# Kernel tuning notes

Hardware: AMD Instinct MI355X
Metric: run time of the kernel (lower is better)

## Reference

```python
import jax, jax.numpy as jnp
import numpy as np

B, NQ, NK, QS, KS, H, VD = 16, 64, 512, 256, 256, 256, 256


def setup_inputs() -> dict:
    key = jax.random.key(0)
    k1, k2, k3, k4, k5, k6, k7 = jax.random.split(key, 7)
    return {
        "queries": jax.random.normal(k1, (B, NQ, QS), dtype=jnp.float32),
        "keys": jax.random.normal(k2, (B, NK, KS), dtype=jnp.float32),
        "values": jax.random.normal(k3, (B, NK, VD), dtype=jnp.float32),
        "valid_lens": jax.random.randint(k4, (B,), 1, NK + 1, dtype=jnp.int32),
        # learned params (nn.Linear with bias=False): W_q [QS,H], W_k [KS,H], w_v [H]
        "W_q": jax.random.normal(k5, (QS, H), dtype=jnp.float32) / np.sqrt(QS),
        "W_k": jax.random.normal(k6, (KS, H), dtype=jnp.float32) / np.sqrt(KS),
        "w_v": jax.random.normal(k7, (H,), dtype=jnp.float32) / np.sqrt(H),
    }


def reference(queries, keys, values, valid_lens, W_q, W_k, w_v):
    # project: q [B,nq,H], k [B,nk,H]
    q = jnp.einsum("bqd,dh->bqh", queries, W_q)
    k = jnp.einsum("bkd,dh->bkh", keys, W_k)
    # broadcast-add -> tanh -> score reduction via w_v: [B,nq,nk]
    features = jnp.tanh(q[:, :, None, :] + k[:, None, :, :])  # [B,nq,nk,H]
    scores = jnp.einsum("bqkh,h->bqk", features, w_v)
    # masked softmax over keys (positions >= valid_len masked out)
    mask = jnp.arange(scores.shape[-1])[None, None, :] < valid_lens[:, None, None]
    scores = jnp.where(mask, scores, -1e6)
    attn = jax.nn.softmax(scores, axis=-1)
    # weighted sum of values (dropout p=0 / eval mode => identity)
    return jnp.einsum("bqk,bkv->bqv", attn, values)
```

## Files before the change

### kernel.cpp

```cpp
#include <hip/hip_runtime.h>
#include <hip/hip_bf16.h>

#define BB 16
#define NQ 64
#define NK 512
#define HD 256

typedef __attribute__((ext_vector_type(8))) short short8;
typedef __attribute__((ext_vector_type(4))) float f32x4;

__device__ __forceinline__ ushort bf16_rne(float v) {
    unsigned u = __float_as_uint(v);
    return (ushort)((u + 0x7FFFu + ((u >> 16) & 1u)) >> 16);
}
__device__ __forceinline__ float bf16_to_f(ushort h) {
    return __uint_as_float(((unsigned)h) << 16);
}

__global__ __launch_bounds__(256) void wconv(
    const float* __restrict__ wq, const float* __restrict__ wk,
    ushort* __restrict__ wqh, ushort* __restrict__ wql,
    ushort* __restrict__ wkh, ushort* __restrict__ wkl)
{
    int widx = blockIdx.x * 256 + threadIdx.x;
    const float* W; ushort *wh, *wl;
    if (widx < 16384) { W = wq; wh = wqh; wl = wql; }
    else { W = wk; wh = wkh; wl = wkl; widx -= 16384; }
    int n  = widx >> 6;
    int k4 = (widx & 63) * 4;
    ushort hh[4], ll[4];
    #pragma unroll
    for (int c = 0; c < 4; ++c) {
        float v = W[(k4 + c) * 256 + n];
        hh[c] = bf16_rne(v);
        ll[c] = bf16_rne(v - bf16_to_f(hh[c]));
    }
    *(ushort4*)&wh[n * 256 + k4] = make_ushort4(hh[0], hh[1], hh[2], hh[3]);
    *(ushort4*)&wl[n * 256 + k4] = make_ushort4(ll[0], ll[1], ll[2], ll[3]);
}

__global__ __launch_bounds__(256, 2) void proj_fused(
    const float* __restrict__ queries, const float* __restrict__ keys,
    const ushort* __restrict__ wqh, const ushort* __restrict__ wql,
    const ushort* __restrict__ wkh, const ushort* __restrict__ wkl,
    float* __restrict__ qp, float* __restrict__ kp, float scale)
{
    __shared__ ushort AsH[64 * 64], AsL[64 * 64];
    __shared__ ushort BsH[64 * 64], BsL[64 * 64];

    const float* A; const ushort *Bh, *Bl; float* C; int rows0;
    const int bx = blockIdx.x;
    if (bx < 16) { A = queries; Bh = wqh; Bl = wql; C = qp; rows0 = bx * 64; }
    else         { A = keys;    Bh = wkh; Bl = wkl; C = kp; rows0 = (bx - 16) * 64; }
    const int cols0 = blockIdx.y * 64;

    const int t = threadIdx.x, lane = t & 63, wave = t >> 6;
    const int quad = lane >> 4, l15 = lane & 15;
    const int sr  = t >> 2;
    const int sc2 = (t & 3) * 2;

    f32x4 acc[4];
    #pragma unroll
    for (int j = 0; j < 4; ++j) acc[j] = (f32x4){0.f, 0.f, 0.f, 0.f};

    for (int k0 = 0; k0 < 256; k0 += 64) {
        const float* arow = &A[(size_t)(rows0 + sr) * 256 + k0 + sc2 * 8];
        float4 a0 = *(const float4*)&arow[0];
        float4 a1 = *(const float4*)&arow[4];
        float4 a2 = *(const float4*)&arow[8];
        float4 a3 = *(const float4*)&arow[12];
        const ushort* bhp = &Bh[(size_t)(cols0 + sr) * 256 + k0 + sc2 * 8];
        const ushort* blp = &Bl[(size_t)(cols0 + sr) * 256 + k0 + sc2 * 8];
        short8 b0h = *(const short8*)&bhp[0];
        short8 b1h = *(const short8*)&bhp[8];
        short8 b0l = *(const short8*)&blp[0];
        short8 b1l = *(const short8*)&blp[8];

        __syncthreads();

        float av[16] = {a0.x, a0.y, a0.z, a0.w, a1.x, a1.y, a1.z, a1.w,
                        a2.x, a2.y, a2.z, a2.w, a3.x, a3.y, a3.z, a3.w};
        short8 ah0, ah1, al0, al1;
        #pragma unroll
        for (int e = 0; e < 8; ++e) {
            ushort h0 = bf16_rne(av[e]);
            ushort h1 = bf16_rne(av[8 + e]);
            ah0[e] = (short)h0;
            ah1[e] = (short)h1;
            al0[e] = (short)bf16_rne(av[e] - bf16_to_f(h0));
            al1[e] = (short)bf16_rne(av[8 + e] - bf16_to_f(h1));
        }
        {
            int s0 = sr * 8 + ((sc2 + 0) ^ (sr & 7));
            int s1 = sr * 8 + ((sc2 + 1) ^ (sr & 7));
            *(short8*)&AsH[s0 * 8] = ah0;
            *(short8*)&AsH[s1 * 8] = ah1;
            *(short8*)&AsL[s0 * 8] = al0;
            *(short8*)&AsL[s1 * 8] = al1;
            *(short8*)&BsH[s0 * 8] = b0h;
            *(short8*)&BsH[s1 * 8] = b1h;
            *(short8*)&BsL[s0 * 8] = b0l;
            *(short8*)&BsL[s1 * 8] = b1l;
        }
        __syncthreads();

        #pragma unroll
        for (int ks = 0; ks < 2; ++ks) {
            const int c = ks * 4 + quad;
            short8 aH, aL, bH[4], bL[4];
            {
                int r = wave * 16 + l15;
                int slot = r * 8 + (c ^ (r & 7));
                aH = *(const short8*)&AsH[slot * 8];
                aL = *(const short8*)&AsL[slot * 8];
            }
            #pragma unroll
            for (int ns = 0; ns < 4; ++ns) {
                int n = ns * 16 + l15;
                int slot = n * 8 + (c ^ (n & 7));
                bH[ns] = *(const short8*)&BsH[slot * 8];
                bL[ns] = *(const short8*)&BsL[slot * 8];
            }
            #pragma unroll
            for (int ns = 0; ns < 4; ++ns)
                acc[ns] = __builtin_amdgcn_mfma_f32_16x16x32_bf16(aH, bH[ns], acc[ns], 0, 0, 0);
            #pragma unroll
            for (int ns = 0; ns < 4; ++ns)
                acc[ns] = __builtin_amdgcn_mfma_f32_16x16x32_bf16(aL, bH[ns], acc[ns], 0, 0, 0);
            #pragma unroll
            for (int ns = 0; ns < 4; ++ns)
                acc[ns] = __builtin_amdgcn_mfma_f32_16x16x32_bf16(aH, bL[ns], acc[ns], 0, 0, 0);
        }
    }

    const int rbase = rows0 + wave * 16 + quad * 4;
    #pragma unroll
    for (int ns = 0; ns < 4; ++ns) {
        int col = cols0 + ns * 16 + l15;
        #pragma unroll
        for (int r = 0; r < 4; ++r)
            C[(size_t)(rbase + r) * 256 + col] =
                __builtin_amdgcn_exp2f(acc[ns][r] * scale);
    }
}

__global__ __launch_bounds__(256, 4) void score_a(
    const float* __restrict__ qp,
    const float* __restrict__ kp,
    const int*   __restrict__ vlens,
    const float* __restrict__ w_v,
    float* __restrict__ Pt)
{
    __shared__ float eq[8][260];
    __shared__ float wv[HD];

    const int b   = blockIdx.x & 15;
    const int qt  = blockIdx.x >> 4;
    const int seg = blockIdx.y;
    const int vl  = vlens[b];
    if (seg * 64 >= vl) return;

    const int t = threadIdx.x, lane = t & 63, wave = t >> 6;
    const int key = wave * 16 + (lane >> 2);
    const int ch  = lane & 3;
    const int kg  = seg * 64 + key;

    const float* krow = kp + ((size_t)b * NK + kg) * HD + ch * 4;
    float4 ek[16];
    #pragma unroll
    for (int j = 0; j < 16; ++j) ek[j] = *(const float4*)&krow[j * 16];

    const float* qsrc = qp + ((size_t)b * NQ + qt * 8) * HD;
    #pragma unroll
    for (int i = 0; i < 2; ++i) {
        int idx = i * 256 + t;
        int row = idx >> 6, c4 = (idx & 63) * 4;
        *(float4*)&eq[row][c4] = *(const float4*)&qsrc[(size_t)row * HD + c4];
    }
    if (t < 64) *(float4*)&wv[t * 4] = *(const float4*)&w_v[t * 4];
    __syncthreads();

    float Wsum;
    {
        float ws = wv[lane] + wv[lane + 64] + wv[lane + 128] + wv[lane + 192];
        #pragma unroll
        for (int off = 32; off; off >>= 1) ws += __shfl_xor(ws, off);
        Wsum = ws;
    }

    float s[8] = {0.f, 0.f, 0.f, 0.f, 0.f, 0.f, 0.f, 0.f};
    #pragma unroll
    for (int j = 0; j < 16; ++j) {
        const int h = j * 16 + ch * 4;
        float4 e4 = ek[j];
        float4 w4 = *(const float4*)&wv[h];
        #pragma unroll
        for (int qi = 0; qi < 8; ++qi) {
            float4 q4 = *(const float4*)&eq[qi][h];
            float p0 = fmaf(q4.x, e4.x, 1.f);
            float p1 = fmaf(q4.y, e4.y, 1.f);
            float p2 = fmaf(q4.z, e4.z, 1.f);
            float p3 = fmaf(q4.w, e4.w, 1.f);
            float d01 = p0 * p1;
            float d23 = p2 * p3;
            float n01 = fmaf(w4.x, p1, w4.y * p0);
            float n23 = fmaf(w4.z, p3, w4.w * p2);
            float num = fmaf(d01, n23, d23 * n01);
            float r   = __builtin_amdgcn_rcpf(d01 * d23);
            s[qi] = fmaf(num, r, s[qi]);
        }
    }
    #pragma unroll
    for (int qi = 0; qi < 8; ++qi) {
        s[qi] += __shfl_xor(s[qi], 1);
        s[qi] += __shfl_xor(s[qi], 2);
    }

    if (ch == 0) {
        const bool masked = (kg >= vl);
        const float L2E = 1.4426950408889634f;
        float pt[8];
        #pragma unroll
        for (int qi = 0; qi < 8; ++qi) {
            float sv = fmaf(-2.f, s[qi], Wsum);
            pt[qi] = masked ? 0.f : __builtin_amdgcn_exp2f(sv * L2E);
        }
        float* dst = &Pt[((size_t)b * NK + kg) * 64 + qt * 8];
        *(float4*)&dst[0] = make_float4(pt[0], pt[1], pt[2], pt[3]);
        *(float4*)&dst[4] = make_float4(pt[4], pt[5], pt[6], pt[7]);
    }
}

__global__ __launch_bounds__(256) void pv_b(
    const float* __restrict__ Pt,
    const float* __restrict__ values,
    const int*   __restrict__ vlens,
    float* __restrict__ out)
{
    __shared__ f32x4 red[128];
    __shared__ float Lred[8];
    __shared__ float Lfin[8];

    const int bx  = blockIdx.x;
    const int b   = bx & 15;
    const int qt  = (bx >> 4) & 7;
    const int vdq = bx >> 7;
    const int vl  = vlens[b];
    const int nk  = ((vl + 63) >> 6) << 6;

    const int t   = threadIdx.x;
    const int vd4 = t & 15;
    const int q   = (t >> 4) & 7;
    const int kp2 = t >> 7;

    const float* vptr = values + (size_t)b * NK * HD + vdq * 64 + vd4 * 4;
    const float* pptr = Pt + (size_t)b * NK * 64 + qt * 8 + q;

    f32x4 acc = (f32x4){0.f, 0.f, 0.f, 0.f};
    float Lacc = 0.f;
    #pragma unroll 8
    for (int k = kp2; k < nk; k += 2) {
        float  p = pptr[(size_t)k * 64];
        float4 v = *(const float4*)&vptr[(size_t)k * HD];
        acc[0] = fmaf(p, v.x, acc[0]);
        acc[1] = fmaf(p, v.y, acc[1]);
        acc[2] = fmaf(p, v.z, acc[2]);
        acc[3] = fmaf(p, v.w, acc[3]);
        Lacc += p;
    }

    if (kp2 == 1) {
        red[t - 128] = acc;
        if (vd4 == 0) Lred[q] = Lacc;
    }
    __syncthreads();
    if (kp2 == 0) {
        f32x4 o = red[t];
        acc[0] += o[0]; acc[1] += o[1]; acc[2] += o[2]; acc[3] += o[3];
        if (vd4 == 0) Lfin[q] = Lacc + Lred[q];
    }
    __syncthreads();
    if (kp2 == 0) {
        float r = __builtin_amdgcn_rcpf(Lfin[q]);
        float4 o = make_float4(acc[0] * r, acc[1] * r, acc[2] * r, acc[3] * r);
        *(float4*)&out[((size_t)(b * 64 + qt * 8 + q)) * 256 + vdq * 64 + vd4 * 4] = o;
    }
}

extern "C" void kernel_launch(void* const* d_in, const int* in_sizes, int n_in,
                              void* d_out, int out_size, void* d_ws, size_t ws_size,
                              hipStream_t stream) {
    const float* queries = (const float*)d_in[0];
    const float* keys    = (const float*)d_in[1];
    const float* values  = (const float*)d_in[2];
    const int*   vlens   = (const int*)d_in[3];
    const float* W_q     = (const float*)d_in[4];
    const float* W_k     = (const float*)d_in[5];
    const float* w_v     = (const float*)d_in[6];
    float* out = (float*)d_out;

    float*  kp  = (float*)d_ws;
    float*  qp  = kp + (size_t)BB * NK * HD;
    float*  Pt  = qp + (size_t)BB * NQ * HD;
    ushort* wqh = (ushort*)(Pt + (size_t)BB * NK * 64);
    ushort* wql = wqh + 65536;
    ushort* wkh = wql + 65536;
    ushort* wkl = wkh + 65536;

    const float SC = 2.885390081777927f;

    wconv<<<dim3(128), 256, 0, stream>>>(W_q, W_k, wqh, wql, wkh, wkl);
    proj_fused<<<dim3(144, 4), 256, 0, stream>>>(queries, keys,
                                                 wqh, wql, wkh, wkl,
                                                 qp, kp, SC);
    score_a<<<dim3(128, 8), 256, 0, stream>>>(qp, kp, vlens, w_v, Pt);
    pv_b<<<dim3(512), 256, 0, stream>>>(Pt, values, vlens, out);
}
```

Baseline: 123.0 us.

## Fuse weight bf16 split into projection GEMM and software-pipeline PV loads

Removes the separate wconv launch. The projection kernel now reads fp32 W_q/W_k directly with strided loads and splits them into bf16 hi/lo inside the tile-staging step. This saves a kernel launch and a workspace round-trip, but each of the 144x4 blocks redoes the conversion and uses uncoalesced column reads of W. Separately, the PV kernel's loop is rewritten as a register double-buffered pipeline that prefetches 8 rows of P and V ahead, to hide global load latency.

```diff
diff --git a/kernel.cpp b/kernel.cpp
--- a/kernel.cpp
+++ b/kernel.cpp
@@ -17,41 +17,18 @@
     return __uint_as_float(((unsigned)h) << 16);
 }
 
-__global__ __launch_bounds__(256) void wconv(
-    const float* __restrict__ wq, const float* __restrict__ wk,
-    ushort* __restrict__ wqh, ushort* __restrict__ wql,
-    ushort* __restrict__ wkh, ushort* __restrict__ wkl)
-{
-    int widx = blockIdx.x * 256 + threadIdx.x;
-    const float* W; ushort *wh, *wl;
-    if (widx < 16384) { W = wq; wh = wqh; wl = wql; }
-    else { W = wk; wh = wkh; wl = wkl; widx -= 16384; }
-    int n  = widx >> 6;
-    int k4 = (widx & 63) * 4;
-    ushort hh[4], ll[4];
-    #pragma unroll
-    for (int c = 0; c < 4; ++c) {
-        float v = W[(k4 + c) * 256 + n];
-        hh[c] = bf16_rne(v);
-        ll[c] = bf16_rne(v - bf16_to_f(hh[c]));
-    }
-    *(ushort4*)&wh[n * 256 + k4] = make_ushort4(hh[0], hh[1], hh[2], hh[3]);
-    *(ushort4*)&wl[n * 256 + k4] = make_ushort4(ll[0], ll[1], ll[2], ll[3]);
-}
-
-__global__ __launch_bounds__(256, 2) void proj_fused(
+__global__ __launch_bounds__(256, 2) void proj_fused2(
     const float* __restrict__ queries, const float* __restrict__ keys,
-    const ushort* __restrict__ wqh, const ushort* __restrict__ wql,
-    const ushort* __restrict__ wkh, const ushort* __restrict__ wkl,
+    const float* __restrict__ W_q, const float* __restrict__ W_k,
     float* __restrict__ qp, float* __restrict__ kp, float scale)
 {
     __shared__ ushort AsH[64 * 64], AsL[64 * 64];
     __shared__ ushort BsH[64 * 64], BsL[64 * 64];
 
-    const float* A; const ushort *Bh, *Bl; float* C; int rows0;
+    const float* A; const float* W; float* C; int rows0;
     const int bx = blockIdx.x;
-    if (bx < 16) { A = queries; Bh = wqh; Bl = wql; C = qp; rows0 = bx * 64; }
-    else         { A = keys;    Bh = wkh; Bl = wkl; C = kp; rows0 = (bx - 16) * 64; }
+    if (bx < 16) { A = queries; W = W_q; C = qp; rows0 = bx * 64; }
+    else         { A = keys;    W = W_k; C = kp; rows0 = (bx - 16) * 64; }
     const int cols0 = blockIdx.y * 64;
 
     const int t = threadIdx.x, lane = t & 63, wave = t >> 6;
@@ -69,18 +46,19 @@
         float4 a1 = *(const float4*)&arow[4];
         float4 a2 = *(const float4*)&arow[8];
         float4 a3 = *(const float4*)&arow[12];
-        const ushort* bhp = &Bh[(size_t)(cols0 + sr) * 256 + k0 + sc2 * 8];
-        const ushort* blp = &Bl[(size_t)(cols0 + sr) * 256 + k0 + sc2 * 8];
-        short8 b0h = *(const short8*)&bhp[0];
-        short8 b1h = *(const short8*)&bhp[8];
-        short8 b0l = *(const short8*)&blp[0];
-        short8 b1l = *(const short8*)&blp[8];
+        float wvv[16];
+        {
+            const float* wsrc = &W[(size_t)(k0 + sc2 * 8) * 256 + cols0 + sr];
+            #pragma unroll
+            for (int e = 0; e < 16; ++e)
+                wvv[e] = wsrc[(size_t)e * 256];
+        }
 
         __syncthreads();
 
         float av[16] = {a0.x, a0.y, a0.z, a0.w, a1.x, a1.y, a1.z, a1.w,
                         a2.x, a2.y, a2.z, a2.w, a3.x, a3.y, a3.z, a3.w};
-        short8 ah0, ah1, al0, al1;
+        short8 ah0, ah1, al0, al1, bh0, bh1, bl0, bl1;
         #pragma unroll
         for (int e = 0; e < 8; ++e) {
             ushort h0 = bf16_rne(av[e]);
@@ -89,6 +67,12 @@
             ah1[e] = (short)h1;
             al0[e] = (short)bf16_rne(av[e] - bf16_to_f(h0));
             al1[e] = (short)bf16_rne(av[8 + e] - bf16_to_f(h1));
+            ushort w0 = bf16_rne(wvv[e]);
+            ushort w1 = bf16_rne(wvv[8 + e]);
+            bh0[e] = (short)w0;
+            bh1[e] = (short)w1;
+            bl0[e] = (short)bf16_rne(wvv[e] - bf16_to_f(w0));
+            bl1[e] = (short)bf16_rne(wvv[8 + e] - bf16_to_f(w1));
         }
         {
             int s0 = sr * 8 + ((sc2 + 0) ^ (sr & 7));
@@ -97,10 +81,10 @@
             *(short8*)&AsH[s1 * 8] = ah1;
             *(short8*)&AsL[s0 * 8] = al0;
             *(short8*)&AsL[s1 * 8] = al1;
-            *(short8*)&BsH[s0 * 8] = b0h;
-            *(short8*)&BsH[s1 * 8] = b1h;
-            *(short8*)&BsL[s0 * 8] = b0l;
-            *(short8*)&BsL[s1 * 8] = b1l;
+            *(short8*)&BsH[s0 * 8] = bh0;
+            *(short8*)&BsH[s1 * 8] = bh1;
+            *(short8*)&BsL[s0 * 8] = bl0;
+            *(short8*)&BsL[s1 * 8] = bl1;
         }
         __syncthreads();
 
@@ -231,7 +215,7 @@
     }
 }
 
-__global__ __launch_bounds__(256) void pv_b(
+__global__ __launch_bounds__(256) void pv_b2(
     const float* __restrict__ Pt,
     const float* __restrict__ values,
     const int*   __restrict__ vlens,
@@ -258,15 +242,36 @@
 
     f32x4 acc = (f32x4){0.f, 0.f, 0.f, 0.f};
     float Lacc = 0.f;
-    #pragma unroll 8
-    for (int k = kp2; k < nk; k += 2) {
-        float  p = pptr[(size_t)k * 64];
-        float4 v = *(const float4*)&vptr[(size_t)k * HD];
-        acc[0] = fmaf(p, v.x, acc[0]);
-        acc[1] = fmaf(p, v.y, acc[1]);
-        acc[2] = fmaf(p, v.z, acc[2]);
-        acc[3] = fmaf(p, v.w, acc[3]);
-        Lacc += p;
+
+    const int iters = nk >> 1;
+    float4 vr[8];
+    float  pr[8];
+    #pragma unroll
+    for (int i = 0; i < 8; ++i) {
+        int k = kp2 + 2 * i;
+        pr[i] = pptr[(size_t)k * 64];
+        vr[i] = *(const float4*)&vptr[(size_t)k * HD];
+    }
+    int base = 8;
+    while (true) {
+        const bool more = base < iters;
+        #pragma unroll
+        for (int i = 0; i < 8; ++i) {
+            float  p = pr[i];
+            float4 v = vr[i];
+            if (more) {
+                int k = kp2 + 2 * (base + i);
+                pr[i] = pptr[(size_t)k * 64];
+                vr[i] = *(const float4*)&vptr[(size_t)k * HD];
+            }
+            acc[0] = fmaf(p, v.x, acc[0]);
+            acc[1] = fmaf(p, v.y, acc[1]);
+            acc[2] = fmaf(p, v.z, acc[2]);
+            acc[3] = fmaf(p, v.w, acc[3]);
+            Lacc += p;
+        }
+        if (!more) break;
+        base += 8;
     }
 
     if (kp2 == 1) {
@@ -299,20 +304,14 @@
     const float* w_v     = (const float*)d_in[6];
     float* out = (float*)d_out;
 
-    float*  kp  = (float*)d_ws;
-    float*  qp  = kp + (size_t)BB * NK * HD;
-    float*  Pt  = qp + (size_t)BB * NQ * HD;
-    ushort* wqh = (ushort*)(Pt + (size_t)BB * NK * 64);
-    ushort* wql = wqh + 65536;
-    ushort* wkh = wql + 65536;
-    ushort* wkl = wkh + 65536;
+    float* kp = (float*)d_ws;
+    float* qp = kp + (size_t)BB * NK * HD;
+    float* Pt = qp + (size_t)BB * NQ * HD;
 
     const float SC = 2.885390081777927f;
 
-    wconv<<<dim3(128), 256, 0, stream>>>(W_q, W_k, wqh, wql, wkh, wkl);
-    proj_fused<<<dim3(144, 4), 256, 0, stream>>>(queries, keys,
-                                                 wqh, wql, wkh, wkl,
-                                                 qp, kp, SC);
+    proj_fused2<<<dim3(144, 4), 256, 0, stream>>>(queries, keys, W_q, W_k,
+                                                  qp, kp, SC);
     score_a<<<dim3(128, 8), 256, 0, stream>>>(qp, kp, vlens, w_v, Pt);
-    pv_b<<<dim3(512), 256, 0, stream>>>(Pt, values, vlens, out);
-}
+    pv_b2<<<dim3(512), 256, 0, stream>>>(Pt, values, vlens, out);
+}
```

Result: slower. 161.5 us (+31.3%).
